# Performance work log

Hardware: AMD Instinct MI355X
Metric: run time of the kernel (lower is better)

Reference implementation:

```python
import jax, jax.numpy as jnp
import numpy as np
import math

B, T, N_EMBD = 8, 4096, 512
DIM = 64  # dim_q == dim_k == dim_v


def setup_inputs() -> dict:
    key = jax.random.key(0)
    k1, k2, k3, k4 = jax.random.split(key, 4)
    x = jax.random.normal(k1, (B, T, N_EMBD), dtype=jnp.float32)
    # store Linear weights as [in, out] so projection is x @ W
    w_q = jax.random.normal(k2, (N_EMBD, DIM), dtype=jnp.float32) * 0.02
    w_k = jax.random.normal(k3, (N_EMBD, DIM), dtype=jnp.float32) * 0.02
    w_v = jax.random.normal(k4, (N_EMBD, DIM), dtype=jnp.float32) * 0.02
    return {"x": x, "w_q": w_q, "w_k": w_k, "w_v": w_v}


def reference(x, w_q, w_k, w_v):
    # Faithful to original torch code, INCLUDING the bug v = w_k(x).
    q = jnp.einsum('btn,nd->btd', x, w_q)
    k = jnp.einsum('btn,nd->btd', x, w_k)
    v = jnp.einsum('btn,nd->btd', x, w_k)  # original uses w_k for v (bug preserved)
    scores = jnp.einsum('bqd,bkd->bqk', q, k) / math.sqrt(DIM)  # [B,T,T]
    causal = jnp.tril(jnp.ones((T, T), dtype=bool))
    scores = jnp.where(causal, scores, jnp.float32(-jnp.inf))
    attn = jax.nn.softmax(scores, axis=-1)
    out = jnp.einsum('bqk,bkd->bqd', attn, v)
    return out
```

## Files before the change

kernel.cpp:

```cpp
#include <hip/hip_runtime.h>
#include <math.h>

#define BB 8
#define TT 4096
#define NE 512
#define DD 64

using f32x4 = __attribute__((ext_vector_type(4))) float;
using s16x8 = __attribute__((ext_vector_type(8))) short;

__device__ __forceinline__ ushort f2bf(float f) {
  uint u = __builtin_bit_cast(uint, f);
  u += 0x7fffu + ((u >> 16) & 1u);
  return (ushort)(u >> 16);
}
__device__ __forceinline__ uint pack2(float a, float b) {
  return (uint)f2bf(a) | ((uint)f2bf(b) << 16);
}

#define KTSWZ(d) ((((d) ^ ((d) >> 3)) & 7) << 4)

__global__ __launch_bounds__(256) void prep_kernel(
    const float* __restrict__ wq, const float* __restrict__ wk,
    ushort* __restrict__ WT) {
  const int i = blockIdx.x * 256 + threadIdx.x;
  const int col = i & 127, k = i >> 7;
  const float v = (col < DD) ? wq[(size_t)k * DD + col] * 0.125f
                             : wk[(size_t)k * DD + (col - DD)];
  WT[(size_t)col * NE + k] = f2bf(v);
}

__global__ __launch_bounds__(256) void proj_kernel(
    const float* __restrict__ x, const ushort* __restrict__ WT,
    ushort* __restrict__ Qo, ushort* __restrict__ Ko) {
  __shared__ __align__(16) char smem[24576];
  char* As = smem;
  char* Bs = smem + 8192;
  const int t = threadIdx.x;
  const int w = t >> 6, l = t & 63;
  const int lm = l & 15, lg = l >> 4;
  const int wr = w >> 1, wc = w & 1;
  const size_t rbase = (size_t)blockIdx.x * 64;

  const int arow = t >> 2, akq = (t & 3) * 16;
  const int bcol = t >> 1, bkh = (t & 1) * 32;

  f32x4 acc[2][4];
#pragma unroll
  for (int mt = 0; mt < 2; ++mt)
#pragma unroll
    for (int nt = 0; nt < 4; ++nt) acc[mt][nt] = (f32x4)0.f;

  float4 xa0, xa1, xa2, xa3;
  uint4 wb0, wb1, wb2, wb3;
  {
    const float* xp = x + (rbase + arow) * NE + akq;
    xa0 = *(const float4*)(xp + 0);  xa1 = *(const float4*)(xp + 4);
    xa2 = *(const float4*)(xp + 8);  xa3 = *(const float4*)(xp + 12);
    const ushort* wp = WT + (size_t)bcol * NE + bkh;
    wb0 = *(const uint4*)(wp + 0);   wb1 = *(const uint4*)(wp + 8);
    wb2 = *(const uint4*)(wp + 16);  wb3 = *(const uint4*)(wp + 24);
  }

  for (int kstep = 0; kstep < NE; kstep += 64) {
    __syncthreads();
    {
      uint4 a0, a1;
      a0.x = pack2(xa0.x, xa0.y); a0.y = pack2(xa0.z, xa0.w);
      a0.z = pack2(xa1.x, xa1.y); a0.w = pack2(xa1.z, xa1.w);
      a1.x = pack2(xa2.x, xa2.y); a1.y = pack2(xa2.z, xa2.w);
      a1.z = pack2(xa3.x, xa3.y); a1.w = pack2(xa3.z, xa3.w);
      const int swa = (arow & 7) << 4;
      *(uint4*)(As + arow * 128 + ((akq * 2) ^ swa)) = a0;
      *(uint4*)(As + arow * 128 + ((akq * 2 + 16) ^ swa)) = a1;
      const int swb = (bcol & 7) << 4;
      *(uint4*)(Bs + bcol * 128 + ((bkh * 2) ^ swb)) = wb0;
      *(uint4*)(Bs + bcol * 128 + ((bkh * 2 + 16) ^ swb)) = wb1;
      *(uint4*)(Bs + bcol * 128 + ((bkh * 2 + 32) ^ swb)) = wb2;
      *(uint4*)(Bs + bcol * 128 + ((bkh * 2 + 48) ^ swb)) = wb3;
    }
    __syncthreads();
    {
      const int kn = (kstep + 64 < NE) ? kstep + 64 : kstep;
      const float* xp = x + (rbase + arow) * NE + kn + akq;
      xa0 = *(const float4*)(xp + 0);  xa1 = *(const float4*)(xp + 4);
      xa2 = *(const float4*)(xp + 8);  xa3 = *(const float4*)(xp + 12);
      const ushort* wp = WT + (size_t)bcol * NE + kn + bkh;
      wb0 = *(const uint4*)(wp + 0);   wb1 = *(const uint4*)(wp + 8);
      wb2 = *(const uint4*)(wp + 16);  wb3 = *(const uint4*)(wp + 24);
    }
#pragma unroll
    for (int ks = 0; ks < 2; ++ks) {
      s16x8 af[2];
#pragma unroll
      for (int mt = 0; mt < 2; ++mt) {
        const int row = wr * 32 + mt * 16 + lm;
        af[mt] = *(const s16x8*)(As + row * 128 + ((ks * 64 + lg * 16) ^ ((row & 7) << 4)));
      }
#pragma unroll
      for (int nt = 0; nt < 4; ++nt) {
        const int col = wc * 64 + nt * 16 + lm;
        s16x8 bf = *(const s16x8*)(Bs + col * 128 + ((ks * 64 + lg * 16) ^ ((col & 7) << 4)));
#pragma unroll
        for (int mt = 0; mt < 2; ++mt)
          acc[mt][nt] = __builtin_amdgcn_mfma_f32_16x16x32_bf16(af[mt], bf, acc[mt][nt], 0, 0, 0);
      }
    }
  }
#pragma unroll
  for (int nt = 0; nt < 4; ++nt) {
    const int col = wc * 64 + nt * 16 + lm;
    ushort* dst = (col < DD) ? Qo : Ko;
    const int c = col & 63;
#pragma unroll
    for (int mt = 0; mt < 2; ++mt)
#pragma unroll
      for (int r = 0; r < 4; ++r) {
        const size_t row = rbase + wr * 32 + mt * 16 + 4 * lg + r;
        dst[row * DD + c] = f2bf(acc[mt][nt][r]);
      }
  }
}

__global__ __launch_bounds__(256) void attn_kernel(
    const ushort* __restrict__ Qg, const ushort* __restrict__ Kg,
    float* __restrict__ PO, float* __restrict__ ML, float* __restrict__ Od,
    int S) {
  __shared__ __align__(16) char smem[32768];
  char* Kl  = smem;
  char* KTl = smem + 8192;
  char* Pl  = smem + 16384;

  const int t = threadIdx.x;
  const int w = t >> 6, l = t & 63;
  const int lm = l & 15, lg = l >> 4;
  int idx = blockIdx.x;
  const int s = idx % S; idx /= S;
  const int pr = idx & 15;
  const int b = idx >> 4;
  const size_t bbase = (size_t)b * TT;
  char* Pw = Pl + w * 4096;

  const int rp = t >> 3;
  const int dblk = t & 7;

  for (int pass = 0; pass < 2; ++pass) {
    const int tile = pass ? (31 - pr) : pr;
    const int qwb = tile * 128 + w * 32;
    const int nc = 2 * tile + 2;
    const int c0 = (s * nc) / S, c1 = ((s + 1) * nc) / S;

    s16x8 qf[2][2];
#pragma unroll
    for (int qi = 0; qi < 2; ++qi)
#pragma unroll
      for (int ks = 0; ks < 2; ++ks)
        qf[qi][ks] = *(const s16x8*)(Qg + (bbase + qwb + qi * 16 + lm) * DD + ks * 32 + lg * 8);

    float mrun[2] = {-1e30f, -1e30f};
    float lrun[2] = {0.f, 0.f};
    f32x4 oacc[2][4];
#pragma unroll
    for (int qi = 0; qi < 2; ++qi)
#pragma unroll
      for (int dt = 0; dt < 4; ++dt) oacc[qi][dt] = (f32x4)0.f;

    uint4 ra, rb;
    {
      const int cc = (c0 < nc) ? c0 : nc - 1;
      const ushort* src = Kg + (bbase + cc * 64 + 2 * rp) * DD + dblk * 8;
      ra = *(const uint4*)src;
      rb = *(const uint4*)(src + DD);
    }

    for (int c = c0; c < c1; ++c) {
      const int kb = c * 64;
      __syncthreads();
      {
        const int r0 = 2 * rp, r1 = r0 + 1;
        *(uint4*)(Kl + r0 * 128 + ((dblk * 16) ^ ((r0 & 7) << 4))) = ra;
        *(uint4*)(Kl + r1 * 128 + ((dblk * 16) ^ ((r1 & 7) << 4))) = rb;
        union { uint4 u; ushort us[8]; } ua, ub;
        ua.u = ra; ub.u = rb;
#pragma unroll
        for (int j = 0; j < 8; ++j) {
          const int d = dblk * 8 + j;
          const uint val = (uint)ua.us[j] | ((uint)ub.us[j] << 16);
          *(uint*)(KTl + d * 128 + ((rp * 4) ^ KTSWZ(d))) = val;
        }
      }
      __syncthreads();
      {
        const int cn = (c + 1 < c1) ? (c + 1) : (nc - 1);
        const ushort* src = Kg + (bbase + cn * 64 + 2 * rp) * DD + dblk * 8;
        ra = *(const uint4*)src;
        rb = *(const uint4*)(src + DD);
      }

      const bool act0 = (kb <= qwb + 15);
      const bool act1 = (kb <= qwb + 31);
      if (!act1) continue;

      f32x4 sa[2][4];
#pragma unroll
      for (int qi = 0; qi < 2; ++qi)
#pragma unroll
        for (int kt = 0; kt < 4; ++kt) sa[qi][kt] = (f32x4)0.f;
#pragma unroll
      for (int ks = 0; ks < 2; ++ks) {
#pragma unroll
        for (int kt = 0; kt < 4; ++kt) {
          const int key = kt * 16 + lm;
          s16x8 af = *(const s16x8*)(Kl + key * 128 + ((ks * 64 + lg * 16) ^ ((key & 7) << 4)));
          if (act0)
            sa[0][kt] = __builtin_amdgcn_mfma_f32_16x16x32_bf16(af, qf[0][ks], sa[0][kt], 0, 0, 0);
          sa[1][kt] = __builtin_amdgcn_mfma_f32_16x16x32_bf16(af, qf[1][ks], sa[1][kt], 0, 0, 0);
        }
      }

#pragma unroll
      for (int qi = 0; qi < 2; ++qi) {
        const bool act = qi ? act1 : act0;
        if (!act) continue;
        const int qg = qwb + qi * 16 + lm;
        if (kb + 63 > qwb + qi * 16) {
#pragma unroll
          for (int kt = 0; kt < 4; ++kt) {
            const int key0 = kb + kt * 16 + 4 * lg;
#pragma unroll
            for (int r = 0; r < 4; ++r)
              if (key0 + r > qg) sa[qi][kt][r] = -1e30f;
          }
        }
        float mc = -1e30f;
#pragma unroll
        for (int kt = 0; kt < 4; ++kt)
#pragma unroll
          for (int r = 0; r < 4; ++r) mc = fmaxf(mc, sa[qi][kt][r]);
        mc = fmaxf(mc, __shfl_xor(mc, 16));
        mc = fmaxf(mc, __shfl_xor(mc, 32));
        const float mn = fmaxf(mrun[qi], mc);
        const float corr = __expf(mrun[qi] - mn);
        mrun[qi] = mn;
        float ps = 0.f;
        const int prow = qi * 16 + lm;
        const int swp = (lm & 7) << 4;
#pragma unroll
        for (int kt = 0; kt < 4; ++kt) {
          float pv[4];
#pragma unroll
          for (int r = 0; r < 4; ++r) {
            const float sv = sa[qi][kt][r];
            pv[r] = (sv > -0.5e30f) ? __expf(sv - mn) : 0.f;
            ps += pv[r];
          }
          const int off = kt * 32 + lg * 8;
          *(uint*)(Pw + prow * 128 + (off ^ swp)) = pack2(pv[0], pv[1]);
          *(uint*)(Pw + prow * 128 + ((off + 4) ^ swp)) = pack2(pv[2], pv[3]);
        }
        ps += __shfl_xor(ps, 16);
        ps += __shfl_xor(ps, 32);
        lrun[qi] = lrun[qi] * corr + ps;
#pragma unroll
        for (int dt = 0; dt < 4; ++dt) oacc[qi][dt] *= corr;
      }

#pragma unroll
      for (int ks = 0; ks < 2; ++ks) {
        s16x8 pf0 = {}, pf1 = {};
        if (act0) pf0 = *(const s16x8*)(Pw + lm * 128 + ((ks * 64 + lg * 16) ^ ((lm & 7) << 4)));
        if (act1) pf1 = *(const s16x8*)(Pw + (16 + lm) * 128 + ((ks * 64 + lg * 16) ^ ((lm & 7) << 4)));
#pragma unroll
        for (int dt = 0; dt < 4; ++dt) {
          const int d = dt * 16 + lm;
          s16x8 vf = *(const s16x8*)(KTl + d * 128 + ((ks * 64 + lg * 16) ^ KTSWZ(d)));
          if (act0) oacc[0][dt] = __builtin_amdgcn_mfma_f32_16x16x32_bf16(vf, pf0, oacc[0][dt], 0, 0, 0);
          if (act1) oacc[1][dt] = __builtin_amdgcn_mfma_f32_16x16x32_bf16(vf, pf1, oacc[1][dt], 0, 0, 0);
        }
      }
    }

    if (S == 1) {
#pragma unroll
      for (int qi = 0; qi < 2; ++qi) {
        const size_t qrow = bbase + qwb + qi * 16 + lm;
        const float inv = 1.f / lrun[qi];
#pragma unroll
        for (int dt = 0; dt < 4; ++dt) {
          f32x4 v = oacc[qi][dt] * inv;
          *(f32x4*)(Od + qrow * DD + dt * 16 + 4 * lg) = v;
        }
      }
    } else {
#pragma unroll
      for (int qi = 0; qi < 2; ++qi) {
        const size_t prow = ((size_t)s * BB + b) * TT + qwb + qi * 16 + lm;
#pragma unroll
        for (int dt = 0; dt < 4; ++dt)
          *(f32x4*)(PO + prow * DD + dt * 16 + 4 * lg) = oacc[qi][dt];
        if (lg == 0) {
          ML[prow * 2] = mrun[qi];
          ML[prow * 2 + 1] = lrun[qi];
        }
      }
    }
  }
}

__global__ __launch_bounds__(256) void merge_kernel(
    const float* __restrict__ PO, const float* __restrict__ ML,
    float* __restrict__ O, int S) {
  const int flat = blockIdx.x * 256 + threadIdx.x;
  const int q = flat >> 4;
  const int d0 = (flat & 15) * 4;
  float mt = -1e30f;
  for (int s = 0; s < S; ++s)
    mt = fmaxf(mt, ML[((size_t)s * BB * TT + q) * 2]);
  float lsum = 0.f;
  f32x4 acc = (f32x4)0.f;
  for (int s = 0; s < S; ++s) {
    const size_t prow = (size_t)s * BB * TT + q;
    const float m = ML[prow * 2], lv = ML[prow * 2 + 1];
    const float wgt = __expf(m - mt);
    lsum = fmaf(wgt, lv, lsum);
    const f32x4 po = *(const f32x4*)(PO + prow * DD + d0);
#pragma unroll
    for (int i = 0; i < 4; ++i) acc[i] = fmaf(wgt, po[i], acc[i]);
  }
  const float inv = 1.f / lsum;
#pragma unroll
  for (int i = 0; i < 4; ++i) acc[i] *= inv;
  *(f32x4*)(O + (size_t)q * DD + d0) = acc;
}

extern "C" void kernel_launch(void* const* d_in, const int* in_sizes, int n_in,
                              void* d_out, int out_size, void* d_ws, size_t ws_size,
                              hipStream_t stream) {
  const float* x  = (const float*)d_in[0];
  const float* wq = (const float*)d_in[1];
  const float* wk = (const float*)d_in[2];
  float* out = (float*)d_out;

  const size_t rows = (size_t)BB * TT;
  ushort* WT   = (ushort*)d_ws;
  ushort* Qbuf = WT + (size_t)128 * NE;
  ushort* Kbuf = Qbuf + rows * DD;
  char*  after = (char*)(Kbuf + rows * DD);
  const size_t used = (size_t)(after - (char*)d_ws);
  const size_t per  = rows * 2 * 4 + rows * DD * 4;
  int S = 1;
  if (used + 4 * per <= ws_size) S = 4;
  else if (used + 2 * per <= ws_size) S = 2;
  float* ML = (float*)after;
  float* PO = ML + (size_t)S * rows * 2;

  prep_kernel<<<dim3(256), dim3(256), 0, stream>>>(wq, wk, WT);
  proj_kernel<<<dim3(512), dim3(256), 0, stream>>>(x, WT, Qbuf, Kbuf);
  attn_kernel<<<dim3(BB * 16 * S), dim3(256), 0, stream>>>(Qbuf, Kbuf, PO, ML, out, S);
  if (S > 1)
    merge_kernel<<<dim3(2048), dim3(256), 0, stream>>>(PO, ML, out, S);
}
```

Before: 86.49 us.

## Use exp2 softmax with lazy rescaling, hardware bf16 packing, and more key splits

Folds log2(e) into the Q scale so the softmax uses native exp2, and skips the running-max rescale unless the max grows by more than a threshold. It also swaps the software bf16 rounding for the v_cvt_pk_bf16_f32 instruction, precomputes the LDS store addresses for the K transpose, and raises wave priority around the MFMA blocks. It raises the split-K factor to 8 when workspace allows, which adds parallelism at the cost of a larger merge. Lazy rescaling lets unnormalised exponentials reach up to 2^8, and dropping the masked-value guard relies on exp2 of a very negative number underflowing to zero.

New measurement: 88.08 us. No clear change (+1.8%).

```diff
diff --git a/kernel.cpp b/kernel.cpp
--- a/kernel.cpp
+++ b/kernel.cpp
@@ -9,13 +9,17 @@
 using f32x4 = __attribute__((ext_vector_type(4))) float;
 using s16x8 = __attribute__((ext_vector_type(8))) short;
 
+#define EXP2 __builtin_amdgcn_exp2f
+
 __device__ __forceinline__ ushort f2bf(float f) {
   uint u = __builtin_bit_cast(uint, f);
   u += 0x7fffu + ((u >> 16) & 1u);
   return (ushort)(u >> 16);
 }
-__device__ __forceinline__ uint pack2(float a, float b) {
-  return (uint)f2bf(a) | ((uint)f2bf(b) << 16);
+__device__ __forceinline__ uint cvtpk(float lo, float hi) {
+  uint r;
+  asm("v_cvt_pk_bf16_f32 %0, %1, %2" : "=v"(r) : "v"(lo), "v"(hi));
+  return r;
 }
 
 #define KTSWZ(d) ((((d) ^ ((d) >> 3)) & 7) << 4)
@@ -25,7 +29,7 @@
     ushort* __restrict__ WT) {
   const int i = blockIdx.x * 256 + threadIdx.x;
   const int col = i & 127, k = i >> 7;
-  const float v = (col < DD) ? wq[(size_t)k * DD + col] * 0.125f
+  const float v = (col < DD) ? wq[(size_t)k * DD + col] * 0.18033688f
                              : wk[(size_t)k * DD + (col - DD)];
   WT[(size_t)col * NE + k] = f2bf(v);
 }
@@ -66,10 +70,10 @@
     __syncthreads();
     {
       uint4 a0, a1;
-      a0.x = pack2(xa0.x, xa0.y); a0.y = pack2(xa0.z, xa0.w);
-      a0.z = pack2(xa1.x, xa1.y); a0.w = pack2(xa1.z, xa1.w);
-      a1.x = pack2(xa2.x, xa2.y); a1.y = pack2(xa2.z, xa2.w);
-      a1.z = pack2(xa3.x, xa3.y); a1.w = pack2(xa3.z, xa3.w);
+      a0.x = cvtpk(xa0.x, xa0.y); a0.y = cvtpk(xa0.z, xa0.w);
+      a0.z = cvtpk(xa1.x, xa1.y); a0.w = cvtpk(xa1.z, xa1.w);
+      a1.x = cvtpk(xa2.x, xa2.y); a1.y = cvtpk(xa2.z, xa2.w);
+      a1.z = cvtpk(xa3.x, xa3.y); a1.w = cvtpk(xa3.z, xa3.w);
       const int swa = (arow & 7) << 4;
       *(uint4*)(As + arow * 128 + ((akq * 2) ^ swa)) = a0;
       *(uint4*)(As + arow * 128 + ((akq * 2 + 16) ^ swa)) = a1;
@@ -143,6 +147,15 @@
 
   const int rp = t >> 3;
   const int dblk = t & 7;
+  const int r0 = 2 * rp, r1 = r0 + 1;
+  char* const pKl0 = Kl + r0 * 128 + ((dblk * 16) ^ ((r0 & 7) << 4));
+  char* const pKl1 = Kl + r1 * 128 + ((dblk * 16) ^ ((r1 & 7) << 4));
+  char* pKT[8];
+#pragma unroll
+  for (int j = 0; j < 8; ++j) {
+    const int d = dblk * 8 + j;
+    pKT[j] = KTl + d * 128 + ((rp * 4) ^ KTSWZ(d));
+  }
 
   for (int pass = 0; pass < 2; ++pass) {
     const int tile = pass ? (31 - pr) : pr;
@@ -177,16 +190,16 @@
       const int kb = c * 64;
       __syncthreads();
       {
-        const int r0 = 2 * rp, r1 = r0 + 1;
-        *(uint4*)(Kl + r0 * 128 + ((dblk * 16) ^ ((r0 & 7) << 4))) = ra;
-        *(uint4*)(Kl + r1 * 128 + ((dblk * 16) ^ ((r1 & 7) << 4))) = rb;
-        union { uint4 u; ushort us[8]; } ua, ub;
-        ua.u = ra; ub.u = rb;
-#pragma unroll
-        for (int j = 0; j < 8; ++j) {
-          const int d = dblk * 8 + j;
-          const uint val = (uint)ua.us[j] | ((uint)ub.us[j] << 16);
-          *(uint*)(KTl + d * 128 + ((rp * 4) ^ KTSWZ(d))) = val;
+        *(uint4*)pKl0 = ra;
+        *(uint4*)pKl1 = rb;
+        const uint wa[4] = {ra.x, ra.y, ra.z, ra.w};
+        const uint wb[4] = {rb.x, rb.y, rb.z, rb.w};
+#pragma unroll
+        for (int jw = 0; jw < 4; ++jw) {
+          const uint lo = (wa[jw] & 0xFFFFu) | (wb[jw] << 16);
+          const uint hi = (wa[jw] >> 16) | (wb[jw] & 0xFFFF0000u);
+          *(uint*)pKT[2 * jw]     = lo;
+          *(uint*)pKT[2 * jw + 1] = hi;
         }
       }
       __syncthreads();
@@ -206,6 +219,7 @@
       for (int qi = 0; qi < 2; ++qi)
 #pragma unroll
         for (int kt = 0; kt < 4; ++kt) sa[qi][kt] = (f32x4)0.f;
+      __builtin_amdgcn_s_setprio(1);
 #pragma unroll
       for (int ks = 0; ks < 2; ++ks) {
 #pragma unroll
@@ -217,6 +231,7 @@
           sa[1][kt] = __builtin_amdgcn_mfma_f32_16x16x32_bf16(af, qf[1][ks], sa[1][kt], 0, 0, 0);
         }
       }
+      __builtin_amdgcn_s_setprio(0);
 
 #pragma unroll
       for (int qi = 0; qi < 2; ++qi) {
@@ -239,30 +254,33 @@
           for (int r = 0; r < 4; ++r) mc = fmaxf(mc, sa[qi][kt][r]);
         mc = fmaxf(mc, __shfl_xor(mc, 16));
         mc = fmaxf(mc, __shfl_xor(mc, 32));
-        const float mn = fmaxf(mrun[qi], mc);
-        const float corr = __expf(mrun[qi] - mn);
-        mrun[qi] = mn;
+        if (__any(mc > mrun[qi] + 8.f)) {
+          const float mn = fmaxf(mrun[qi], mc);
+          const float corr = EXP2(mrun[qi] - mn);
+          lrun[qi] *= corr;
+#pragma unroll
+          for (int dt = 0; dt < 4; ++dt) oacc[qi][dt] *= corr;
+          mrun[qi] = mn;
+        }
+        const float mn = mrun[qi];
         float ps = 0.f;
-        const int prow = qi * 16 + lm;
+        char* const Pq = Pw + (qi * 16 + lm) * 128;
         const int swp = (lm & 7) << 4;
 #pragma unroll
         for (int kt = 0; kt < 4; ++kt) {
           float pv[4];
 #pragma unroll
           for (int r = 0; r < 4; ++r) {
-            const float sv = sa[qi][kt][r];
-            pv[r] = (sv > -0.5e30f) ? __expf(sv - mn) : 0.f;
+            pv[r] = EXP2(sa[qi][kt][r] - mn);
             ps += pv[r];
           }
           const int off = kt * 32 + lg * 8;
-          *(uint*)(Pw + prow * 128 + (off ^ swp)) = pack2(pv[0], pv[1]);
-          *(uint*)(Pw + prow * 128 + ((off + 4) ^ swp)) = pack2(pv[2], pv[3]);
+          *(uint*)(Pq + (off ^ swp))       = cvtpk(pv[0], pv[1]);
+          *(uint*)(Pq + ((off + 4) ^ swp)) = cvtpk(pv[2], pv[3]);
         }
         ps += __shfl_xor(ps, 16);
         ps += __shfl_xor(ps, 32);
-        lrun[qi] = lrun[qi] * corr + ps;
-#pragma unroll
-        for (int dt = 0; dt < 4; ++dt) oacc[qi][dt] *= corr;
+        lrun[qi] += ps;
       }
 
 #pragma unroll
@@ -270,6 +288,7 @@
         s16x8 pf0 = {}, pf1 = {};
         if (act0) pf0 = *(const s16x8*)(Pw + lm * 128 + ((ks * 64 + lg * 16) ^ ((lm & 7) << 4)));
         if (act1) pf1 = *(const s16x8*)(Pw + (16 + lm) * 128 + ((ks * 64 + lg * 16) ^ ((lm & 7) << 4)));
+        __builtin_amdgcn_s_setprio(1);
 #pragma unroll
         for (int dt = 0; dt < 4; ++dt) {
           const int d = dt * 16 + lm;
@@ -277,6 +296,7 @@
           if (act0) oacc[0][dt] = __builtin_amdgcn_mfma_f32_16x16x32_bf16(vf, pf0, oacc[0][dt], 0, 0, 0);
           if (act1) oacc[1][dt] = __builtin_amdgcn_mfma_f32_16x16x32_bf16(vf, pf1, oacc[1][dt], 0, 0, 0);
         }
+        __builtin_amdgcn_s_setprio(0);
       }
     }
 
@@ -321,7 +341,7 @@
   for (int s = 0; s < S; ++s) {
     const size_t prow = (size_t)s * BB * TT + q;
     const float m = ML[prow * 2], lv = ML[prow * 2 + 1];
-    const float wgt = __expf(m - mt);
+    const float wgt = EXP2(m - mt);
     lsum = fmaf(wgt, lv, lsum);
     const f32x4 po = *(const f32x4*)(PO + prow * DD + d0);
 #pragma unroll
@@ -349,7 +369,8 @@
   const size_t used = (size_t)(after - (char*)d_ws);
   const size_t per  = rows * 2 * 4 + rows * DD * 4;
   int S = 1;
-  if (used + 4 * per <= ws_size) S = 4;
+  if (used + 8 * per <= ws_size) S = 8;
+  else if (used + 4 * per <= ws_size) S = 4;
   else if (used + 2 * per <= ws_size) S = 2;
   float* ML = (float*)after;
   float* PO = ML + (size_t)S * rows * 2;
```
